# Performance work log

Measured on AMD Instinct MI355X. Metric: run time of the kernel, lower is better.

## Reference

```python
import jax, jax.numpy as jnp
import numpy as np

N_NODES = 100000
N_EDGES = 3200000
N_HID = 3
HEAD_OUT = 1024


def setup_inputs() -> dict:
    key = jax.random.key(0)
    ks = jax.random.split(key, 8)
    feat1 = jax.random.normal(ks[0], (N_NODES, 1), dtype=jnp.float32)
    feat2 = jax.random.normal(ks[1], (N_NODES, 1), dtype=jnp.float32)
    norm = jax.random.uniform(ks[2], (N_EDGES,), dtype=jnp.float32)
    src = jax.random.randint(ks[3], (N_EDGES,), 0, N_NODES, dtype=jnp.int32)
    dst = jax.random.randint(ks[4], (N_EDGES,), 0, N_NODES, dtype=jnp.int32)
    # per-layer GIN apply_func Linear(1,1): weight [n_hid,1,1], bias [n_hid,1]
    gin_w = jax.random.normal(ks[5], (N_HID, 1, 1), dtype=jnp.float32)
    gin_b = jax.random.normal(ks[6], (N_HID, 1), dtype=jnp.float32) * 0.1
    # head Linear(num_nodes, 1024), stored as [in, out]
    net_w = jax.random.normal(ks[7], (N_NODES, HEAD_OUT), dtype=jnp.float32) * (1.0 / np.sqrt(N_NODES))
    net_b = jnp.zeros((HEAD_OUT,), dtype=jnp.float32)
    return {"feat1": feat1, "feat2": feat2, "norm": norm, "src": src, "dst": dst,
            "gin_w": gin_w, "gin_b": gin_b, "net_w": net_w, "net_b": net_b}


def reference(feat1, feat2, norm, src, dst, gin_w, gin_b, net_w, net_b):
    n = feat1.shape[0]
    e_dtype = feat1.dtype
    # in-degree (same every layer); DGL mean over mailbox divides by in-degree
    deg = jax.ops.segment_sum(jnp.ones((src.shape[0],), e_dtype), dst, num_segments=n)
    inv_deg = (1.0 / jnp.maximum(deg, 1.0))[:, None]  # [N,1]

    def forward_each(feat):
        x = feat  # [N,1]
        saved = []
        for l in range(gin_w.shape[0]):
            msg = x[src] * norm[:, None]                                # gather + edge weight [E,1]
            agg = jax.ops.segment_sum(msg, dst, num_segments=n) * inv_deg  # mean aggregate [N,1]
            rst = (x + agg) @ gin_w[l].T + gin_b[l]                     # GIN: (1+eps)*x + agg, eps=0, then Linear
            saved.append(rst)                                           # forward hook captures pre-relu output
            x = jax.nn.relu(rst)
        feats = jnp.mean(jnp.stack(saved), axis=0)  # mean over layers [N,1]
        h = feats.reshape(1, -1)                    # flatten -> [1, N]
        return h @ net_w + net_b                    # [1, 1024]

    x1 = forward_each(feat1)
    x2 = forward_each(feat2)
    return jax.nn.sigmoid(jnp.sum(x1 * x2, axis=1, keepdims=True))  # [1,1]
```

## Files before the change

### kernel.cpp

```cpp
#include <hip/hip_runtime.h>
#include <math.h>

static constexpr int NN  = 100000;
static constexpr int NE  = 3200000;
static constexpr int HO  = 1024;
static constexpr int BSH = 5;
static constexpr int BMASK = 31;
static constexpr int NB  = 3125;
static constexpr int NBP = NB + 1;
static constexpr int PB  = 256;
static constexpr int CHUNK = NE / PB;
static constexpr int AT  = 512;
static constexpr int PER_A = (NB + AT - 1) / AT;
static constexpr int RPB = 100;
static constexpr int HB  = NN / RPB;
static constexpr int CAP = 2048;
static constexpr int BT  = 49;

typedef float f4v __attribute__((ext_vector_type(4)));

__device__ __forceinline__ int bucket_swz(int blk) {
    int x = blk & 7, g = blk >> 3;
    return (x < 5) ? x * 391 + g : 1955 + (x - 5) * 390 + g;
}

__global__ void init_k(const float* __restrict__ f1, const float* __restrict__ f2,
                       float2* __restrict__ x0, float* __restrict__ xacc,
                       int* __restrict__ nodeoff) {
    int i = blockIdx.x * 256 + threadIdx.x;
    if (i < NN) x0[i] = make_float2(f1[i], f2[i]);
    if (i < 2 * HO) xacc[i] = 0.f;
    if (i == 0) nodeoff[NN] = NE;
}

__global__ __launch_bounds__(AT) void partA_k(const int* __restrict__ src,
                                              const int* __restrict__ dst,
                                              const float* __restrict__ norm,
                                              int* __restrict__ loffg,
                                              uint2* __restrict__ blocked) {
    __shared__ int hist[NB];
    __shared__ int scanbuf[AT];
    int blk = blockIdx.x, t = threadIdx.x;
    for (int i = t; i < NB; i += AT) hist[i] = 0;
    __syncthreads();
    int base = blk * CHUNK;
    for (int i = t; i < CHUNK; i += AT)
        atomicAdd(&hist[dst[base + i] >> BSH], 1);
    __syncthreads();
    int loc[PER_A]; int s = 0;
    int b0 = t * PER_A;
    for (int k = 0; k < PER_A; ++k) {
        int i = b0 + k;
        int v = (i < NB) ? hist[i] : 0;
        loc[k] = s; s += v;
    }
    scanbuf[t] = s; __syncthreads();
    for (int off = 1; off < AT; off <<= 1) {
        int v = (t >= off) ? scanbuf[t - off] : 0; __syncthreads();
        scanbuf[t] += v; __syncthreads();
    }
    int carry = t ? scanbuf[t - 1] : 0;
    for (int k = 0; k < PER_A; ++k) {
        int i = b0 + k;
        if (i < NB) {
            int e = carry + loc[k];
            loffg[blk * NBP + i] = e;
            hist[i] = e;
        }
    }
    __syncthreads();
    for (int i = t; i < CHUNK; i += AT) {
        int e = base + i;
        int d = dst[e];
        int pos = atomicAdd(&hist[d >> BSH], 1);
        blocked[base + pos] = make_uint2((unsigned)src[e] | ((unsigned)(d & BMASK) << 17),
                                         __float_as_uint(norm[e]));
    }
}

__global__ __launch_bounds__(256) void transT_k(const int* __restrict__ loffg,
                                                int* __restrict__ loffT) {
    __shared__ int tile[64][65];
    int bx = blockIdx.x % BT;
    int ky = blockIdx.x / BT;
    int tx = threadIdx.x & 63, ty = threadIdx.x >> 6;
    int b = bx * 64 + tx;
#pragma unroll
    for (int j = 0; j < 16; ++j) {
        int k = ky * 64 + ty + j * 4;
        tile[ty + j * 4][tx] = (b < NB) ? loffg[k * NBP + b] : 0;
    }
    __syncthreads();
#pragma unroll
    for (int j = 0; j < 16; ++j) {
        int row = ty + j * 4;
        int bb = bx * 64 + row;
        if (bb < NB) loffT[bb * PB + ky * 64 + tx] = tile[tx][row];
    }
}

__global__ __launch_bounds__(256) void sortB_k(const uint2* __restrict__ blocked,
                                               const int* __restrict__ loffT,
                                               uint2* __restrict__ sorted2,
                                               int* __restrict__ nodeoff) {
    __shared__ uint2 rec[CAP];
    __shared__ int runoff[256];
    __shared__ int cnt[32], cur[32], preoff[32];
    __shared__ float inv[32];
    __shared__ int s0sh;
    int t = threadIdx.x;
    int b = bucket_swz(blockIdx.x);
    int o0 = loffT[b * PB + t];
    int o1 = (b == NB - 1) ? CHUNK : loffT[(b + 1) * PB + t];
    int len = o1 - o0;
    if (t == 0) s0sh = 0;
    if (t < 32) cnt[t] = 0;
    runoff[t] = len;
    __syncthreads();
    atomicAdd(&s0sh, o0);
    for (int off = 1; off < 256; off <<= 1) {
        int v = (t >= off) ? runoff[t - off] : 0; __syncthreads();
        runoff[t] += v; __syncthreads();
    }
    int start = runoff[t] - len;
    int total = runoff[255];
    if (total > CAP) total = CAP;
    const uint2* srcp = blocked + (size_t)t * CHUNK + o0;
    for (int j = 0; j < len; ++j) {
        int p = start + j;
        if (p < CAP) rec[p] = srcp[j];
    }
    __syncthreads();
    for (int i = t; i < total; i += 256)
        atomicAdd(&cnt[(rec[i].x >> 17) & BMASK], 1);
    __syncthreads();
    if (t == 0) {
        int pre = 0;
        for (int lo = 0; lo < 32; ++lo) {
            int c = cnt[lo];
            preoff[lo] = pre; cur[lo] = pre;
            inv[lo] = 1.0f / fmaxf((float)c, 1.0f);
            pre += c;
        }
    }
    __syncthreads();
    int s0 = s0sh;
    for (int i = t; i < total; i += 256) {
        uint2 r = rec[i];
        int lo = (r.x >> 17) & BMASK;
        int pos = atomicAdd(&cur[lo], 1);
        sorted2[(size_t)s0 + pos] = make_uint2(r.x & 131071u,
                               __float_as_uint(__uint_as_float(r.y) * inv[lo]));
    }
    if (t < 32) nodeoff[(b << BSH) + t] = s0 + preoff[t];
}

template<int L0>
__global__ __launch_bounds__(256) void layer_k(const uint2* __restrict__ s2,
                                               const int* __restrict__ noff,
                                               const float2* __restrict__ xin,
                                               float2* __restrict__ xout,
                                               float2* __restrict__ ssum,
                                               const float* __restrict__ gw,
                                               const float* __restrict__ gb, int l) {
    int gid = blockIdx.x * 256 + threadIdx.x;
    int node = gid >> 3, r = gid & 7;
    if (node >= NN) return;
    int i0 = noff[node], i1 = noff[node + 1];
    float ax = 0.f, ay = 0.f;
    for (int i = i0 + r; i < i1; i += 8) {
        uint2 rec = s2[i];
        float2 xx = xin[rec.x];
        float w = __uint_as_float(rec.y);
        ax = fmaf(xx.x, w, ax); ay = fmaf(xx.y, w, ay);
    }
#pragma unroll
    for (int off = 1; off < 8; off <<= 1) {
        ax += __shfl_xor(ax, off, 64);
        ay += __shfl_xor(ay, off, 64);
    }
    if (r == 0) {
        float w = gw[l], bb = gb[l];
        float2 xv = xin[node];
        float rx = fmaf(xv.x + ax, w, bb);
        float ry = fmaf(xv.y + ay, w, bb);
        if (L0) ssum[node] = make_float2(rx, ry);
        else { float2 s = ssum[node]; ssum[node] = make_float2(s.x + rx, s.y + ry); }
        xout[node] = make_float2(fmaxf(rx, 0.f), fmaxf(ry, 0.f));
    }
}

__global__ __launch_bounds__(256) void head_k(const float2* __restrict__ ssum,
                                              const float* __restrict__ W,
                                              float* __restrict__ part) {
    __shared__ float sf0[RPB], sf1[RPB];
    int r0 = blockIdx.x * RPB;
    int t = threadIdx.x;
    const float sc = 1.0f / 3.0f;
    if (t < RPB) {
        float2 s = ssum[r0 + t];
        sf0[t] = s.x * sc;
        sf1[t] = s.y * sc;
    }
    __syncthreads();
    float ax1=0.f, ay1=0.f, az1=0.f, aw1=0.f;
    float ax2=0.f, ay2=0.f, az2=0.f, aw2=0.f;
    int j0 = t * 4;
    const f4v* Wp = reinterpret_cast<const f4v*>(W + (size_t)r0 * HO + j0);
#pragma unroll 4
    for (int k = 0; k < RPB; ++k) {
        f4v w4 = __builtin_nontemporal_load(Wp);
        Wp += HO / 4;
        float f1 = sf0[k], f2 = sf1[k];
        ax1 = fmaf(f1, w4.x, ax1); ay1 = fmaf(f1, w4.y, ay1);
        az1 = fmaf(f1, w4.z, az1); aw1 = fmaf(f1, w4.w, aw1);
        ax2 = fmaf(f2, w4.x, ax2); ay2 = fmaf(f2, w4.y, ay2);
        az2 = fmaf(f2, w4.z, az2); aw2 = fmaf(f2, w4.w, aw2);
    }
    float* pp = part + (size_t)blockIdx.x * 2048;
    pp[j0]   = ax1; pp[j0+1] = ay1; pp[j0+2] = az1; pp[j0+3] = aw1;
    pp[1024+j0]   = ax2; pp[1024+j0+1] = ay2;
    pp[1024+j0+2] = az2; pp[1024+j0+3] = aw2;
}

__global__ __launch_bounds__(256) void reduce_k(const float* __restrict__ part,
                                                float* __restrict__ xacc) {
    int gid = blockIdx.x * 256 + threadIdx.x;
    int j = gid & 2047;
    int seg = gid >> 11;
    int b0 = (seg * HB) >> 5, b1 = ((seg + 1) * HB) >> 5;
    float s = 0.f;
    for (int b = b0; b < b1; ++b) s += part[(size_t)b * 2048 + j];
    atomicAdd(&xacc[j], s);
}

__global__ void final_k(const float* __restrict__ xacc, const float* __restrict__ nb,
                        float* __restrict__ out) {
    __shared__ float red[256];
    int t = threadIdx.x;
    float v = 0.f;
    for (int j = t; j < HO; j += 256)
        v += (xacc[j] + nb[j]) * (xacc[HO + j] + nb[j]);
    red[t] = v;
    __syncthreads();
    for (int s = 128; s > 0; s >>= 1) {
        if (t < s) red[t] += red[t + s];
        __syncthreads();
    }
    if (t == 0) out[0] = 1.0f / (1.0f + expf(-red[0]));
}

extern "C" void kernel_launch(void* const* d_in, const int* in_sizes, int n_in,
                              void* d_out, int out_size, void* d_ws, size_t ws_size,
                              hipStream_t stream) {
    const float* feat1 = (const float*)d_in[0];
    const float* feat2 = (const float*)d_in[1];
    const float* norm  = (const float*)d_in[2];
    const int*   src   = (const int*)  d_in[3];
    const int*   dst   = (const int*)  d_in[4];
    const float* gin_w = (const float*)d_in[5];
    const float* gin_b = (const float*)d_in[6];
    const float* net_w = (const float*)d_in[7];
    const float* net_b = (const float*)d_in[8];
    float* out = (float*)d_out;

    char* p = (char*)d_ws;
    uint2* blocked = (uint2*)p;               p += (size_t)NE * 8;
    float* part    = (float*)blocked;
    uint2* sorted2 = (uint2*)p;               p += (size_t)NE * 8;
    int*   loffg   = (int*)p;                 p += (size_t)PB * NBP * 4;
    int*   loffT   = (int*)p;                 p += (size_t)NB * PB * 4;
    int*   nodeoff = (int*)p;                 p += ((size_t)(NN + 1) * 4 + 15) & ~15ull;
    float2* x0     = (float2*)p;              p += (size_t)NN * 8;
    float2* x1     = (float2*)p;              p += (size_t)NN * 8;
    float2* ssum   = (float2*)p;              p += (size_t)NN * 8;
    float* xacc    = (float*)p;               p += (size_t)2 * HO * 4;

    int ng = (NN + 255) / 256;
    int lg = (NN * 8 + 255) / 256;

    init_k<<<ng, 256, 0, stream>>>(feat1, feat2, x0, xacc, nodeoff);
    partA_k<<<PB, AT, 0, stream>>>(src, dst, norm, loffg, blocked);
    transT_k<<<BT * 4, 256, 0, stream>>>(loffg, loffT);
    sortB_k<<<NB, 256, 0, stream>>>(blocked, loffT, sorted2, nodeoff);

    layer_k<1><<<lg, 256, 0, stream>>>(sorted2, nodeoff, x0, x1, ssum, gin_w, gin_b, 0);
    layer_k<0><<<lg, 256, 0, stream>>>(sorted2, nodeoff, x1, x0, ssum, gin_w, gin_b, 1);
    layer_k<0><<<lg, 256, 0, stream>>>(sorted2, nodeoff, x0, x1, ssum, gin_w, gin_b, 2);

    head_k<<<HB, 256, 0, stream>>>(ssum, net_w, part);
    reduce_k<<<256, 256, 0, stream>>>(part, xacc);
    final_k<<<1, 256, 0, stream>>>(xacc, net_b, out);
}
```

Baseline: 232.8 us.

## Fuse init into partition, use wave-shuffle scans, unroll gathers, halve head rows

Folds the init kernel into partA_k, removing one launch. Replaces the LDS Hillis-Steele scans in partA_k and sortB_k with wavefront shuffle scans, which need fewer barriers. The sortB_k per-bucket prefix becomes a 32-lane shuffle scan instead of a serial loop on one thread. sortB_k's record copy and layer_k's gather loop are unrolled to put more loads in flight. The head kernel now processes 50 rows per block, doubling the block count and the partial buffer that reduce_k must sum.

```diff
diff --git a/kernel.cpp b/kernel.cpp
--- a/kernel.cpp
+++ b/kernel.cpp
@@ -12,7 +12,7 @@
 static constexpr int CHUNK = NE / PB;
 static constexpr int AT  = 512;
 static constexpr int PER_A = (NB + AT - 1) / AT;
-static constexpr int RPB = 100;
+static constexpr int RPB = 50;
 static constexpr int HB  = NN / RPB;
 static constexpr int CAP = 2048;
 static constexpr int BT  = 49;
@@ -24,23 +24,26 @@
     return (x < 5) ? x * 391 + g : 1955 + (x - 5) * 390 + g;
 }
 
-__global__ void init_k(const float* __restrict__ f1, const float* __restrict__ f2,
-                       float2* __restrict__ x0, float* __restrict__ xacc,
-                       int* __restrict__ nodeoff) {
-    int i = blockIdx.x * 256 + threadIdx.x;
-    if (i < NN) x0[i] = make_float2(f1[i], f2[i]);
-    if (i < 2 * HO) xacc[i] = 0.f;
-    if (i == 0) nodeoff[NN] = NE;
-}
-
-__global__ __launch_bounds__(AT) void partA_k(const int* __restrict__ src,
+__global__ __launch_bounds__(AT) void partA_k(const float* __restrict__ f1,
+                                              const float* __restrict__ f2,
+                                              const int* __restrict__ src,
                                               const int* __restrict__ dst,
                                               const float* __restrict__ norm,
                                               int* __restrict__ loffg,
-                                              uint2* __restrict__ blocked) {
+                                              uint2* __restrict__ blocked,
+                                              float2* __restrict__ x0,
+                                              float* __restrict__ xacc,
+                                              int* __restrict__ nodeoff) {
     __shared__ int hist[NB];
-    __shared__ int scanbuf[AT];
+    __shared__ int wt[8];
     int blk = blockIdx.x, t = threadIdx.x;
+    int lane = t & 63, w = t >> 6;
+    int gi = blk * AT + t;
+    if (gi < NN) x0[gi] = make_float2(f1[gi], f2[gi]);
+    if (blk == 0) {
+        for (int i = t; i < 2 * HO; i += AT) xacc[i] = 0.f;
+        if (t == 0) nodeoff[NN] = NE;
+    }
     for (int i = t; i < NB; i += AT) hist[i] = 0;
     __syncthreads();
     int base = blk * CHUNK;
@@ -49,17 +52,25 @@
     __syncthreads();
     int loc[PER_A]; int s = 0;
     int b0 = t * PER_A;
+#pragma unroll
     for (int k = 0; k < PER_A; ++k) {
         int i = b0 + k;
         int v = (i < NB) ? hist[i] : 0;
         loc[k] = s; s += v;
     }
-    scanbuf[t] = s; __syncthreads();
-    for (int off = 1; off < AT; off <<= 1) {
-        int v = (t >= off) ? scanbuf[t - off] : 0; __syncthreads();
-        scanbuf[t] += v; __syncthreads();
-    }
-    int carry = t ? scanbuf[t - 1] : 0;
+    int incl = s;
+#pragma unroll
+    for (int off = 1; off < 64; off <<= 1) {
+        int v = __shfl_up(incl, off, 64);
+        if (lane >= off) incl += v;
+    }
+    if (lane == 63) wt[w] = incl;
+    __syncthreads();
+    int wpre = 0;
+#pragma unroll
+    for (int k = 0; k < 8; ++k) if (k < w) wpre += wt[k];
+    int carry = wpre + incl - s;
+#pragma unroll
     for (int k = 0; k < PER_A; ++k) {
         int i = b0 + k;
         if (i < NB) {
@@ -104,55 +115,83 @@
                                                uint2* __restrict__ sorted2,
                                                int* __restrict__ nodeoff) {
     __shared__ uint2 rec[CAP];
-    __shared__ int runoff[256];
-    __shared__ int cnt[32], cur[32], preoff[32];
+    __shared__ int wtot[4], wsum[4];
+    __shared__ int cnt[32], curs[32];
     __shared__ float inv[32];
-    __shared__ int s0sh;
     int t = threadIdx.x;
+    int lane = t & 63, w = t >> 6;
     int b = bucket_swz(blockIdx.x);
     int o0 = loffT[b * PB + t];
     int o1 = (b == NB - 1) ? CHUNK : loffT[(b + 1) * PB + t];
     int len = o1 - o0;
-    if (t == 0) s0sh = 0;
     if (t < 32) cnt[t] = 0;
-    runoff[t] = len;
-    __syncthreads();
-    atomicAdd(&s0sh, o0);
-    for (int off = 1; off < 256; off <<= 1) {
-        int v = (t >= off) ? runoff[t - off] : 0; __syncthreads();
-        runoff[t] += v; __syncthreads();
-    }
-    int start = runoff[t] - len;
-    int total = runoff[255];
+    int incl = len;
+#pragma unroll
+    for (int off = 1; off < 64; off <<= 1) {
+        int v = __shfl_up(incl, off, 64);
+        if (lane >= off) incl += v;
+    }
+    int os = o0;
+#pragma unroll
+    for (int off = 32; off; off >>= 1) os += __shfl_xor(os, off, 64);
+    if (lane == 63) wtot[w] = incl;
+    if (lane == 0)  wsum[w] = os;
+    __syncthreads();
+    int wpre = 0, total = 0, s0 = 0;
+#pragma unroll
+    for (int k = 0; k < 4; ++k) {
+        int tv = wtot[k];
+        if (k < w) wpre += tv;
+        total += tv; s0 += wsum[k];
+    }
+    int start = wpre + incl - len;
     if (total > CAP) total = CAP;
-    const uint2* srcp = blocked + (size_t)t * CHUNK + o0;
-    for (int j = 0; j < len; ++j) {
-        int p = start + j;
-        if (p < CAP) rec[p] = srcp[j];
+    {
+        int lm = (len > 0) ? len - 1 : 0;
+        const uint2* srcq = blocked + (size_t)t * CHUNK + o0;
+        uint2 q0 = srcq[0];
+        uint2 q1 = srcq[lm < 1 ? lm : 1];
+        uint2 q2 = srcq[lm < 2 ? lm : 2];
+        uint2 q3 = srcq[lm < 3 ? lm : 3];
+        uint2 q4 = srcq[lm < 4 ? lm : 4];
+        uint2 q5 = srcq[lm < 5 ? lm : 5];
+        uint2 q6 = srcq[lm < 6 ? lm : 6];
+        uint2 q7 = srcq[lm < 7 ? lm : 7];
+        if (len > 0 && start + 0 < CAP) rec[start + 0] = q0;
+        if (len > 1 && start + 1 < CAP) rec[start + 1] = q1;
+        if (len > 2 && start + 2 < CAP) rec[start + 2] = q2;
+        if (len > 3 && start + 3 < CAP) rec[start + 3] = q3;
+        if (len > 4 && start + 4 < CAP) rec[start + 4] = q4;
+        if (len > 5 && start + 5 < CAP) rec[start + 5] = q5;
+        if (len > 6 && start + 6 < CAP) rec[start + 6] = q6;
+        if (len > 7 && start + 7 < CAP) rec[start + 7] = q7;
+        for (int j = 8; j < len; ++j)
+            if (start + j < CAP) rec[start + j] = srcq[j];
     }
     __syncthreads();
     for (int i = t; i < total; i += 256)
         atomicAdd(&cnt[(rec[i].x >> 17) & BMASK], 1);
     __syncthreads();
-    if (t == 0) {
-        int pre = 0;
-        for (int lo = 0; lo < 32; ++lo) {
-            int c = cnt[lo];
-            preoff[lo] = pre; cur[lo] = pre;
-            inv[lo] = 1.0f / fmaxf((float)c, 1.0f);
-            pre += c;
+    if (t < 32) {
+        int c = cnt[t];
+        int ic = c;
+#pragma unroll
+        for (int off = 1; off < 32; off <<= 1) {
+            int v = __shfl_up(ic, off, 32);
+            if (t >= off) ic += v;
         }
-    }
-    __syncthreads();
-    int s0 = s0sh;
+        curs[t] = ic - c;
+        inv[t] = 1.0f / fmaxf((float)c, 1.0f);
+        nodeoff[(b << BSH) + t] = s0 + ic - c;
+    }
+    __syncthreads();
     for (int i = t; i < total; i += 256) {
         uint2 r = rec[i];
         int lo = (r.x >> 17) & BMASK;
-        int pos = atomicAdd(&cur[lo], 1);
+        int pos = atomicAdd(&curs[lo], 1);
         sorted2[(size_t)s0 + pos] = make_uint2(r.x & 131071u,
                                __float_as_uint(__uint_as_float(r.y) * inv[lo]));
     }
-    if (t < 32) nodeoff[(b << BSH) + t] = s0 + preoff[t];
 }
 
 template<int L0>
@@ -168,11 +207,21 @@
     if (node >= NN) return;
     int i0 = noff[node], i1 = noff[node + 1];
     float ax = 0.f, ay = 0.f;
-    for (int i = i0 + r; i < i1; i += 8) {
-        uint2 rec = s2[i];
-        float2 xx = xin[rec.x];
-        float w = __uint_as_float(rec.y);
-        ax = fmaf(xx.x, w, ax); ay = fmaf(xx.y, w, ay);
+    int i = i0 + r;
+    while (i + 24 < i1) {
+        uint2 a0 = s2[i], a1 = s2[i + 8], a2 = s2[i + 16], a3 = s2[i + 24];
+        float2 xa = xin[a0.x], xb = xin[a1.x], xc = xin[a2.x], xd = xin[a3.x];
+        ax = fmaf(xa.x, __uint_as_float(a0.y), ax); ay = fmaf(xa.y, __uint_as_float(a0.y), ay);
+        ax = fmaf(xb.x, __uint_as_float(a1.y), ax); ay = fmaf(xb.y, __uint_as_float(a1.y), ay);
+        ax = fmaf(xc.x, __uint_as_float(a2.y), ax); ay = fmaf(xc.y, __uint_as_float(a2.y), ay);
+        ax = fmaf(xd.x, __uint_as_float(a3.y), ax); ay = fmaf(xd.y, __uint_as_float(a3.y), ay);
+        i += 32;
+    }
+    for (; i < i1; i += 8) {
+        uint2 a = s2[i];
+        float2 xx = xin[a.x];
+        float wv = __uint_as_float(a.y);
+        ax = fmaf(xx.x, wv, ax); ay = fmaf(xx.y, wv, ay);
     }
 #pragma unroll
     for (int off = 1; off < 8; off <<= 1) {
@@ -180,10 +229,10 @@
         ay += __shfl_xor(ay, off, 64);
     }
     if (r == 0) {
-        float w = gw[l], bb = gb[l];
+        float wv = gw[l], bb = gb[l];
         float2 xv = xin[node];
-        float rx = fmaf(xv.x + ax, w, bb);
-        float ry = fmaf(xv.y + ay, w, bb);
+        float rx = fmaf(xv.x + ax, wv, bb);
+        float ry = fmaf(xv.y + ay, wv, bb);
         if (L0) ssum[node] = make_float2(rx, ry);
         else { float2 s = ssum[node]; ssum[node] = make_float2(s.x + rx, s.y + ry); }
         xout[node] = make_float2(fmaxf(rx, 0.f), fmaxf(ry, 0.f));
@@ -207,7 +256,7 @@
     float ax2=0.f, ay2=0.f, az2=0.f, aw2=0.f;
     int j0 = t * 4;
     const f4v* Wp = reinterpret_cast<const f4v*>(W + (size_t)r0 * HO + j0);
-#pragma unroll 4
+#pragma unroll 5
     for (int k = 0; k < RPB; ++k) {
         f4v w4 = __builtin_nontemporal_load(Wp);
         Wp += HO / 4;
@@ -276,11 +325,10 @@
     float2* ssum   = (float2*)p;              p += (size_t)NN * 8;
     float* xacc    = (float*)p;               p += (size_t)2 * HO * 4;
 
-    int ng = (NN + 255) / 256;
     int lg = (NN * 8 + 255) / 256;
 
-    init_k<<<ng, 256, 0, stream>>>(feat1, feat2, x0, xacc, nodeoff);
-    partA_k<<<PB, AT, 0, stream>>>(src, dst, norm, loffg, blocked);
+    partA_k<<<PB, AT, 0, stream>>>(feat1, feat2, src, dst, norm, loffg, blocked,
+                                   x0, xacc, nodeoff);
     transT_k<<<BT * 4, 256, 0, stream>>>(loffg, loffT);
     sortB_k<<<NB, 256, 0, stream>>>(blocked, loffT, sorted2, nodeoff);
 
```

Measured after the change: 226.8 us. -2.6%, faster.
